# Performance work log

Measured on AMD Instinct MI355X. Metric: run time of the kernel, lower is better.

Reference implementation:

```python
import jax, jax.numpy as jnp
import numpy as np

DEPTH = 13                 # tree depth -> N = 2**DEPTH - 1 reaches (heap layout, outlet = node 0)
N = 2 ** DEPTH - 1         # 8191 reaches
T = 2048                   # timesteps


def setup_inputs() -> dict:
    key = jax.random.key(0)
    ks = jax.random.split(key, 8)
    u = lambda k, shape, lo, hi: jax.random.uniform(k, shape, minval=lo, maxval=hi, dtype=jnp.float32)
    return {
        "lateral_inflows": u(ks[0], (T, N), 0.0, 2.0),     # m^3/s lateral inflow per reach
        "manning_n":       u(ks[1], (N,), 0.025, 0.06),    # Manning roughness
        "lengths":         u(ks[2], (N,), 1000.0, 5000.0), # reach length [m]
        "slopes":          u(ks[3], (N,), 1e-4, 1e-2),     # bed slope (>= 1e-4 as in source)
        "width_coefs":     u(ks[4], (N,), 3.0, 10.0),      # w = wc * Q**we  (power-law geometry)
        "width_exps":      u(ks[5], (N,), 0.4, 0.6),
        "depth_coefs":     u(ks[6], (N,), 0.2, 0.5),       # h = dc * Q**de
        "depth_exps":      u(ks[7], (N,), 0.3, 0.45),
        "dt": 3600,                                        # routing timestep [s]
    }


def _mc_outflow(I_new, I_old, O_old, n, L, S, wc, we, dc, de, dt):
    """Variable-parameter Muskingum-Cunge update for one vector of reaches."""
    Qr = jnp.maximum(0.5 * (I_new + O_old), 1e-3)          # reference discharge
    h = dc * Qr ** de                                       # hydraulic depth
    w = wc * Qr ** we                                       # top width
    v = h ** (2.0 / 3.0) * jnp.sqrt(S) / n                  # Manning velocity
    c = jnp.maximum((5.0 / 3.0) * v, 1e-3)                  # kinematic celerity
    K = L / c                                               # travel time
    X = jnp.clip(0.5 * (1.0 - Qr / (w * S * c * L)), 0.0, 0.5)
    den = 2.0 * K * (1.0 - X) + dt
    C1 = (dt - 2.0 * K * X) / den
    C2 = (dt + 2.0 * K * X) / den
    C3 = (2.0 * K * (1.0 - X) - dt) / den
    return jnp.maximum(C1 * I_new + C2 * I_old + C3 * O_old, 0.0)


def reference(lateral_inflows, manning_n, lengths, slopes, width_coefs, width_exps,
              depth_coefs, depth_exps, dt):
    dtf = jnp.float32(dt)
    Np = lateral_inflows.shape[1]
    params = (manning_n, lengths, slopes, width_coefs, width_exps, depth_coefs, depth_exps)

    def step(carry, lat_t):
        I_old, O_old = carry                                # [N] prev inflow / outflow
        Q = jnp.zeros(Np, dtype=lat_t.dtype)                # new outflows this timestep
        I_all = jnp.zeros(Np, dtype=lat_t.dtype)
        # process levels leaves -> root (reverse topological order over the DAG)
        for l in range(DEPTH - 1, -1, -1):
            s, e = 2 ** l - 1, 2 ** (l + 1) - 1             # nodes of level l
            if l == DEPTH - 1:
                up = jnp.float32(0.0)                        # headwater reaches
            else:
                cs, ce = 2 ** (l + 1) - 1, 2 ** (l + 2) - 1  # children = level l+1
                up = Q[cs:ce:2] + Q[cs + 1:ce:2]             # sum of 2 upstream discharges
            I_new = lat_t[s:e] + up
            O_new = _mc_outflow(I_new, I_old[s:e], O_old[s:e],
                                *(p[s:e] for p in params), dtf)
            Q = Q.at[s:e].set(O_new)
            I_all = I_all.at[s:e].set(I_new)
        return (I_all, Q), Q[0]                              # outlet = root (index 0)

    init = (jnp.zeros(Np, jnp.float32), jnp.zeros(Np, jnp.float32))
    _, outlet_Q = jax.lax.scan(step, init, lateral_inflows)
    return outlet_Q                                          # [T]
```

## Files before the change

kernel.cpp:

```cpp
#include <hip/hip_runtime.h>


#define NN 8191
#define TT 2048
#define BATCH 32
#define NBLK 39
#define BTHREADS 256

#define FLAGS_FOFF 16773120ull
#define REQ_BYTES  67106816ull

#if __has_builtin(__builtin_amdgcn_exp2f)
__device__ __forceinline__ float fexp2(float x) { return __builtin_amdgcn_exp2f(x); }
#else
__device__ __forceinline__ float fexp2(float x) { return exp2f(x); }
#endif
#if __has_builtin(__builtin_amdgcn_logf)
__device__ __forceinline__ float flog2(float x) { return __builtin_amdgcn_logf(x); }
#else
__device__ __forceinline__ float flog2(float x) { return log2f(x); }
#endif
#if __has_builtin(__builtin_amdgcn_rcpf)
__device__ __forceinline__ float frcp(float x) { return __builtin_amdgcn_rcpf(x); }
#else
__device__ __forceinline__ float frcp(float x) { return 1.0f / x; }
#endif

__device__ __forceinline__ float mc_update(float Inew, float Iold, float Oold,
                                           float em, float tkc, float ex, float k1,
                                           float dtf)
{
    float Qr = fmaxf(0.5f * (Inew + Oold), 1e-3f);
    float lg = flog2(Qr);
    float twoK = tkc * fexp2(em * lg);
    float X = fmaxf(0.5f - k1 * fexp2(ex * lg), 0.0f);
    float A = twoK * X;
    float B = twoK - A;
    float r = frcp(B + dtf);
    float C1 = (dtf - A) * r;
    float C2 = (dtf + A) * r;
    float C3 = (B - dtf) * r;
    return fmaxf(C1 * Inew + C2 * Iold + C3 * Oold, 0.0f);
}

__constant__ int g_level[NBLK] = {
    12,12,12,12,12,12,12,12,12,12,12,12,12,12,12,12,
    11,11,11,11,11,11,11,11,
    10,10,10,10,
    9,9,
    8,7,6,5,4,3,2,1,0};
__constant__ int g_cnt[NBLK] = {
    256,256,256,256,256,256,256,256,256,256,256,256,256,256,256,256,
    256,256,256,256,256,256,256,256,
    256,256,256,256,
    256,256,
    256,128,64,32,16,8,4,2,1};
__constant__ int g_first[13] = {38,37,36,35,34,33,32,31,30,28,24,16,0};
__constant__ unsigned long long g_off[13] = {
    16773120ull, 16769024ull, 16760832ull, 16744448ull, 16711680ull,
    16646144ull, 16515072ull, 16252928ull, 15728640ull, 14680064ull,
    12582912ull, 8388608ull, 0ull};

#define FLAG_STRIDE 16

__device__ __forceinline__ void waitflags(const unsigned int* fa, const unsigned int* fb,
                                          unsigned int target)
{
    while (true) {
        unsigned int a = __hip_atomic_load(fa, __ATOMIC_RELAXED, __HIP_MEMORY_SCOPE_AGENT);
        unsigned int b = fb ? __hip_atomic_load(fb, __ATOMIC_RELAXED, __HIP_MEMORY_SCOPE_AGENT)
                            : a;
        if (a >= target && b >= target) break;
        __builtin_amdgcn_s_sleep(1);
    }
    __builtin_amdgcn_sched_barrier(0);
    asm volatile("" ::: "memory");
}

__global__ void zero_flags(unsigned int* flags)
{
    for (int i = threadIdx.x; i < NBLK * 4 * FLAG_STRIDE; i += 256) flags[i] = 0;
}

__global__ __launch_bounds__(BTHREADS)
void pipe_kernel(const float* __restrict__ lat,
                 const float* __restrict__ nman,
                 const float* __restrict__ len,
                 const float* __restrict__ slp,
                 const float* __restrict__ wcf,
                 const float* __restrict__ wex,
                 const float* __restrict__ dcf,
                 const float* __restrict__ dex,
                 const int*   __restrict__ dtp,
                 float*       __restrict__ out,
                 float*       __restrict__ ws)
{
    const int bid = blockIdx.x;
    const int tid = threadIdx.x;
    const int lvl = g_level[bid];
    const int cnt = g_cnt[bid];
    const int W   = tid >> 6;
    const int wn  = cnt - W * 64;
    if (wn <= 0) return;

    const bool active = (tid < cnt);
    const int B = bid - g_first[lvl];
    const int m = B * 256 + (active ? tid : 0);
    const int node = ((1 << lvl) - 1) + m;
    const int wbase = B * 256 + W * 64;

    unsigned int* flags = (unsigned int*)(ws + FLAGS_FOFF);
    unsigned int* myflag = flags + ((size_t)bid * 4 + W) * FLAG_STRIDE;

    const bool haschild = (lvl < 12);
    const unsigned int* fa = nullptr;
    const unsigned int* fb = nullptr;
    if (haschild) {
        const int Fp = g_first[lvl + 1];
        const int nw = wn < 64 ? wn : 64;
        const int p0 = (2 * wbase) >> 6;
        const int p1 = (2 * wbase + 2 * nw - 1) >> 6;
        fa = flags + ((size_t)(Fp + (p0 >> 2)) * 4 + (p0 & 3)) * FLAG_STRIDE;
        fb = (p1 != p0)
           ? flags + ((size_t)(Fp + (p1 >> 2)) * 4 + (p1 & 3)) * FLAG_STRIDE
           : nullptr;
    }

    const int myW = 1 << lvl;
    const int childW = 1 << (lvl + 1);
    float* myBuf = ws + g_off[lvl];
    const unsigned long long* childBuf =
        haschild ? (const unsigned long long*)(ws + g_off[lvl + 1]) : nullptr;

    const float dtf = (float)dtp[0];

    float em, tkc, ex, k1;
    float Iold = 0.0f, Oold = 0.0f;
    {
        float n = nman[node], L = len[node], S = slp[node];
        float wc = wcf[node], we = wex[node], dc = dcf[node], de = dex[node];
        float dc23 = fexp2(0.6666667f * flog2(dc));
        float cc = 1.6666667f * dc23 * sqrtf(S) * frcp(n);
        float e23 = 0.6666667f * de;
        em  = -e23;
        tkc = 2.0f * L * frcp(cc);
        ex  = 1.0f - we - e23;
        k1  = 0.5f * frcp(S * L * wc * cc);
    }

    for (int t0 = 0; t0 < TT; t0 += BATCH) {
        float la[BATCH];
        if (active) {
#pragma unroll
            for (int k = 0; k < BATCH; ++k)
                la[k] = lat[(size_t)(t0 + k) * NN + node];
        }

        if (haschild) waitflags(fa, fb, (unsigned int)(t0 + BATCH));

        if (active) {
            float c0[BATCH], c1[BATCH];
            if (haschild) {
#pragma unroll
                for (int k = 0; k < BATCH; ++k) {
                    unsigned long long cv = __hip_atomic_load(
                        childBuf + ((size_t)(t0 + k) * childW >> 1) + m,
                        __ATOMIC_RELAXED, __HIP_MEMORY_SCOPE_AGENT);
                    float2 c = *(float2*)&cv;
                    c0[k] = c.x; c1[k] = c.y;
                }
            }
#pragma unroll
            for (int k = 0; k < BATCH; ++k) {
                float Inew = la[k] + (haschild ? (c0[k] + c1[k]) : 0.0f);
                float O = mc_update(Inew, Iold, Oold, em, tkc, ex, k1, dtf);
                Iold = Inew; Oold = O;
                if (lvl > 0)
                    __hip_atomic_store(myBuf + (size_t)(t0 + k) * myW + m, O,
                                       __ATOMIC_RELAXED, __HIP_MEMORY_SCOPE_AGENT);
                else
                    out[t0 + k] = O;
            }
        }
        if (lvl > 0) {
            asm volatile("s_waitcnt vmcnt(0)" ::: "memory");
            if ((tid & 63) == 0)
                __hip_atomic_store(myflag, (unsigned int)(t0 + BATCH),
                                   __ATOMIC_RELAXED, __HIP_MEMORY_SCOPE_AGENT);
        }
    }
}

#define NTHREADS 1024
__global__ __launch_bounds__(NTHREADS)
void route_kernel(const float* __restrict__ lat,
                  const float* __restrict__ nman,
                  const float* __restrict__ len,
                  const float* __restrict__ slp,
                  const float* __restrict__ wcf,
                  const float* __restrict__ wex,
                  const float* __restrict__ dcf,
                  const float* __restrict__ dex,
                  const int*   __restrict__ dtp,
                  float*       __restrict__ out)
{
    __shared__ float Osh[NN];
    const int tid = threadIdx.x;
    const float dtf = (float)dtp[0];

    int nodes[8];
    nodes[0] = 4095 + tid;
    nodes[1] = 5119 + tid;
    nodes[2] = 6143 + tid;
    nodes[3] = 7167 + tid;
    nodes[4] = 2047 + tid;
    nodes[5] = 3071 + tid;
    nodes[6] = 1023 + tid;
    nodes[7] = (tid < 1023) ? tid : 0;

    float em[8], tkc[8], ex[8], k1[8];
    float Ireg[8], Oreg[8];
#pragma unroll
    for (int k = 0; k < 8; ++k) {
        int i = nodes[k];
        float n = nman[i], L = len[i], S = slp[i];
        float wc = wcf[i], we = wex[i], dc = dcf[i], de = dex[i];
        float dc23 = fexp2(0.6666667f * flog2(dc));
        float cc = 1.6666667f * dc23 * sqrtf(S) * frcp(n);
        float e23 = 0.6666667f * de;
        em[k]  = -e23;
        tkc[k] = 2.0f * L * frcp(cc);
        ex[k]  = 1.0f - we - e23;
        k1[k]  = 0.5f * frcp(S * L * wc * cc);
        Ireg[k] = 0.0f; Oreg[k] = 0.0f;
    }
    for (int i = tid; i < NN; i += NTHREADS) Osh[i] = 0.0f;
    __syncthreads();

    for (int t = 0; t < TT; ++t) {
        const float* __restrict__ latt = lat + (size_t)t * NN;
#pragma unroll
        for (int k = 0; k < 4; ++k) {
            int i = nodes[k];
            float Inew = latt[i];
            float O = mc_update(Inew, Ireg[k], Oreg[k], em[k], tkc[k], ex[k], k1[k], dtf);
            Ireg[k] = Inew; Oreg[k] = O; Osh[i] = O;
        }
        __syncthreads();
#pragma unroll
        for (int k = 4; k < 6; ++k) {
            int i = nodes[k];
            float Inew = latt[i] + Osh[2 * i + 1] + Osh[2 * i + 2];
            float O = mc_update(Inew, Ireg[k], Oreg[k], em[k], tkc[k], ex[k], k1[k], dtf);
            Ireg[k] = Inew; Oreg[k] = O; Osh[i] = O;
        }
        __syncthreads();
        {
            int i = nodes[6];
            float Inew = latt[i] + Osh[2 * i + 1] + Osh[2 * i + 2];
            float O = mc_update(Inew, Ireg[6], Oreg[6], em[6], tkc[6], ex[6], k1[6], dtf);
            Ireg[6] = Inew; Oreg[6] = O; Osh[i] = O;
        }
        __syncthreads();
        for (int l = 9; l >= 0; --l) {
            int s = (1 << l) - 1;
            int e = (1 << (l + 1)) - 1;
            if (tid >= s && tid < e) {
                int i = tid;
                float Inew = latt[i] + Osh[2 * i + 1] + Osh[2 * i + 2];
                float O = mc_update(Inew, Ireg[7], Oreg[7], em[7], tkc[7], ex[7], k1[7], dtf);
                Ireg[7] = Inew; Oreg[7] = O; Osh[i] = O;
            }
            __syncthreads();
        }
        if (tid == 0) out[t] = Oreg[7];
    }
}

extern "C" void kernel_launch(void* const* d_in, const int* in_sizes, int n_in,
                              void* d_out, int out_size, void* d_ws, size_t ws_size,
                              hipStream_t stream) {
    const float* lat  = (const float*)d_in[0];
    const float* nman = (const float*)d_in[1];
    const float* len  = (const float*)d_in[2];
    const float* slp  = (const float*)d_in[3];
    const float* wcf  = (const float*)d_in[4];
    const float* wex  = (const float*)d_in[5];
    const float* dcf  = (const float*)d_in[6];
    const float* dex  = (const float*)d_in[7];
    const int*   dtp  = (const int*)d_in[8];
    float* out = (float*)d_out;

    if (ws_size >= REQ_BYTES) {
        float* ws = (float*)d_ws;
        unsigned int* flags = (unsigned int*)(ws + FLAGS_FOFF);
        zero_flags<<<dim3(1), dim3(256), 0, stream>>>(flags);
        pipe_kernel<<<dim3(NBLK), dim3(BTHREADS), 0, stream>>>(
            lat, nman, len, slp, wcf, wex, dcf, dex, dtp, out, ws);
    } else {
        route_kernel<<<dim3(1), dim3(NTHREADS), 0, stream>>>(
            lat, nman, len, slp, wcf, wex, dcf, dex, dtp, out);
    }
}
```

Measured before the change: 483.5 us.

## Double-buffer lateral and child loads within larger flag batches in pipelined routing kernel

The level-pipelined kernel now waits on child flags once per 128 timesteps instead of every 32. Inside each batch it processes 16-step chunks and prefetches the next chunk's lateral and child values into alternate register buffers while computing the current one. The Muskingum-Cunge output is also rewritten algebraically to skip computing C1/C2/C3 separately. The larger batch cuts synchronization overhead but makes parent levels wait longer to start, which lengthens the pipeline fill across the 13 levels.

Measured after the change: 681.5 us. 1.41x slower.

```diff
diff --git a/kernel.cpp b/kernel.cpp
--- a/kernel.cpp
+++ b/kernel.cpp
@@ -3,12 +3,14 @@
 
 #define NN 8191
 #define TT 2048
-#define BATCH 32
+#define FBATCH 128
+#define CHUNK 16
 #define NBLK 39
 #define BTHREADS 256
 
 #define FLAGS_FOFF 16773120ull
 #define REQ_BYTES  67106816ull
+#define FLAG_STRIDE 16
 
 #if __has_builtin(__builtin_amdgcn_exp2f)
 __device__ __forceinline__ float fexp2(float x) { return __builtin_amdgcn_exp2f(x); }
@@ -25,23 +27,6 @@
 #else
 __device__ __forceinline__ float frcp(float x) { return 1.0f / x; }
 #endif
-
-__device__ __forceinline__ float mc_update(float Inew, float Iold, float Oold,
-                                           float em, float tkc, float ex, float k1,
-                                           float dtf)
-{
-    float Qr = fmaxf(0.5f * (Inew + Oold), 1e-3f);
-    float lg = flog2(Qr);
-    float twoK = tkc * fexp2(em * lg);
-    float X = fmaxf(0.5f - k1 * fexp2(ex * lg), 0.0f);
-    float A = twoK * X;
-    float B = twoK - A;
-    float r = frcp(B + dtf);
-    float C1 = (dtf - A) * r;
-    float C2 = (dtf + A) * r;
-    float C3 = (B - dtf) * r;
-    return fmaxf(C1 * Inew + C2 * Iold + C3 * Oold, 0.0f);
-}
 
 __constant__ int g_level[NBLK] = {
     12,12,12,12,12,12,12,12,12,12,12,12,12,12,12,12,
@@ -61,8 +46,6 @@
     16646144ull, 16515072ull, 16252928ull, 15728640ull, 14680064ull,
     12582912ull, 8388608ull, 0ull};
 
-#define FLAG_STRIDE 16
-
 __device__ __forceinline__ void waitflags(const unsigned int* fa, const unsigned int* fb,
                                           unsigned int target)
 {
@@ -148,50 +131,98 @@
         k1  = 0.5f * frcp(S * L * wc * cc);
     }
 
-    for (int t0 = 0; t0 < TT; t0 += BATCH) {
-        float la[BATCH];
-        if (active) {
-#pragma unroll
-            for (int k = 0; k < BATCH; ++k)
-                la[k] = lat[(size_t)(t0 + k) * NN + node];
-        }
-
-        if (haschild) waitflags(fa, fb, (unsigned int)(t0 + BATCH));
-
-        if (active) {
-            float c0[BATCH], c1[BATCH];
-            if (haschild) {
-#pragma unroll
-                for (int k = 0; k < BATCH; ++k) {
-                    unsigned long long cv = __hip_atomic_load(
-                        childBuf + ((size_t)(t0 + k) * childW >> 1) + m,
-                        __ATOMIC_RELAXED, __HIP_MEMORY_SCOPE_AGENT);
-                    float2 c = *(float2*)&cv;
-                    c0[k] = c.x; c1[k] = c.y;
-                }
-            }
-#pragma unroll
-            for (int k = 0; k < BATCH; ++k) {
-                float Inew = la[k] + (haschild ? (c0[k] + c1[k]) : 0.0f);
-                float O = mc_update(Inew, Iold, Oold, em, tkc, ex, k1, dtf);
-                Iold = Inew; Oold = O;
-                if (lvl > 0)
-                    __hip_atomic_store(myBuf + (size_t)(t0 + k) * myW + m, O,
-                                       __ATOMIC_RELAXED, __HIP_MEMORY_SCOPE_AGENT);
-                else
-                    out[t0 + k] = O;
-            }
-        }
+    float laA[CHUNK], c0A[CHUNK], c1A[CHUNK];
+    float laB[CHUNK], c0B[CHUNK], c1B[CHUNK];
+
+#define LLOAD(buf, tb)                                                        \
+    if (active) {                                                             \
+        _Pragma("unroll")                                                     \
+        for (int k = 0; k < CHUNK; ++k)                                       \
+            buf[k] = lat[(size_t)((tb) + k) * NN + node];                     \
+    }
+
+#define CLOAD(b0, b1, tb)                                                     \
+    if (haschild && active) {                                                 \
+        _Pragma("unroll")                                                     \
+        for (int k = 0; k < CHUNK; ++k) {                                     \
+            unsigned long long cv = __hip_atomic_load(                        \
+                childBuf + ((size_t)((tb) + k) * childW >> 1) + m,            \
+                __ATOMIC_RELAXED, __HIP_MEMORY_SCOPE_AGENT);                  \
+            float2 c = *(float2*)&cv;                                         \
+            b0[k] = c.x; b1[k] = c.y;                                         \
+        }                                                                     \
+    }
+
+#define COMP(la, b0, b1, tb)                                                  \
+    if (active) {                                                             \
+        _Pragma("unroll")                                                     \
+        for (int k = 0; k < CHUNK; ++k) {                                     \
+            float Inew = la[k] + (haschild ? (b0[k] + b1[k]) : 0.0f);         \
+            float Qr = fmaxf(0.5f * (Inew + Oold), 1e-3f);                    \
+            float lg = flog2(Qr);                                             \
+            float twoK = tkc * fexp2(em * lg);                                \
+            float X = fmaxf(0.5f - k1 * fexp2(ex * lg), 0.0f);                \
+            float A = twoK * X;                                               \
+            float Bv = twoK - A;                                              \
+            float r = frcp(Bv + dtf);                                         \
+            float num = dtf * (Inew + Iold - Oold) + A * (Iold - Inew)        \
+                      + Bv * Oold;                                            \
+            float O = fmaxf(num * r, 0.0f);                                   \
+            Iold = Inew; Oold = O;                                            \
+            if (lvl > 0)                                                      \
+                __hip_atomic_store(myBuf + (size_t)((tb) + k) * myW + m, O,   \
+                                   __ATOMIC_RELAXED, __HIP_MEMORY_SCOPE_AGENT);\
+            else                                                              \
+                out[(tb) + k] = O;                                            \
+        }                                                                     \
+    }
+
+    LLOAD(laA, 0);
+
+    for (int t0 = 0; t0 < TT; t0 += FBATCH) {
+        if (haschild) waitflags(fa, fb, (unsigned int)(t0 + FBATCH));
+
+        CLOAD(c0A, c1A, t0);
+        LLOAD(laB, t0 + 16);  CLOAD(c0B, c1B, t0 + 16);  COMP(laA, c0A, c1A, t0);
+        LLOAD(laA, t0 + 32);  CLOAD(c0A, c1A, t0 + 32);  COMP(laB, c0B, c1B, t0 + 16);
+        LLOAD(laB, t0 + 48);  CLOAD(c0B, c1B, t0 + 48);  COMP(laA, c0A, c1A, t0 + 32);
+        LLOAD(laA, t0 + 64);  CLOAD(c0A, c1A, t0 + 64);  COMP(laB, c0B, c1B, t0 + 48);
+        LLOAD(laB, t0 + 80);  CLOAD(c0B, c1B, t0 + 80);  COMP(laA, c0A, c1A, t0 + 64);
+        LLOAD(laA, t0 + 96);  CLOAD(c0A, c1A, t0 + 96);  COMP(laB, c0B, c1B, t0 + 80);
+        LLOAD(laB, t0 + 112); CLOAD(c0B, c1B, t0 + 112); COMP(laA, c0A, c1A, t0 + 96);
+        COMP(laB, c0B, c1B, t0 + 112);
+
         if (lvl > 0) {
             asm volatile("s_waitcnt vmcnt(0)" ::: "memory");
             if ((tid & 63) == 0)
-                __hip_atomic_store(myflag, (unsigned int)(t0 + BATCH),
+                __hip_atomic_store(myflag, (unsigned int)(t0 + FBATCH),
                                    __ATOMIC_RELAXED, __HIP_MEMORY_SCOPE_AGENT);
         }
-    }
+        if (t0 + FBATCH < TT) { LLOAD(laA, t0 + FBATCH); }
+    }
+#undef LLOAD
+#undef CLOAD
+#undef COMP
 }
 
 #define NTHREADS 1024
+__device__ __forceinline__ float mc_update_fb(float Inew, float Iold, float Oold,
+                                              float em, float tkc, float ex, float k1,
+                                              float dtf)
+{
+    float Qr = fmaxf(0.5f * (Inew + Oold), 1e-3f);
+    float lg = flog2(Qr);
+    float twoK = tkc * fexp2(em * lg);
+    float X = fmaxf(0.5f - k1 * fexp2(ex * lg), 0.0f);
+    float A = twoK * X;
+    float B = twoK - A;
+    float r = frcp(B + dtf);
+    float C1 = (dtf - A) * r;
+    float C2 = (dtf + A) * r;
+    float C3 = (B - dtf) * r;
+    return fmaxf(C1 * Inew + C2 * Iold + C3 * Oold, 0.0f);
+}
+
 __global__ __launch_bounds__(NTHREADS)
 void route_kernel(const float* __restrict__ lat,
                   const float* __restrict__ nman,
@@ -243,7 +274,7 @@
         for (int k = 0; k < 4; ++k) {
             int i = nodes[k];
             float Inew = latt[i];
-            float O = mc_update(Inew, Ireg[k], Oreg[k], em[k], tkc[k], ex[k], k1[k], dtf);
+            float O = mc_update_fb(Inew, Ireg[k], Oreg[k], em[k], tkc[k], ex[k], k1[k], dtf);
             Ireg[k] = Inew; Oreg[k] = O; Osh[i] = O;
         }
         __syncthreads();
@@ -251,14 +282,14 @@
         for (int k = 4; k < 6; ++k) {
             int i = nodes[k];
             float Inew = latt[i] + Osh[2 * i + 1] + Osh[2 * i + 2];
-            float O = mc_update(Inew, Ireg[k], Oreg[k], em[k], tkc[k], ex[k], k1[k], dtf);
+            float O = mc_update_fb(Inew, Ireg[k], Oreg[k], em[k], tkc[k], ex[k], k1[k], dtf);
             Ireg[k] = Inew; Oreg[k] = O; Osh[i] = O;
         }
         __syncthreads();
         {
             int i = nodes[6];
             float Inew = latt[i] + Osh[2 * i + 1] + Osh[2 * i + 2];
-            float O = mc_update(Inew, Ireg[6], Oreg[6], em[6], tkc[6], ex[6], k1[6], dtf);
+            float O = mc_update_fb(Inew, Ireg[6], Oreg[6], em[6], tkc[6], ex[6], k1[6], dtf);
             Ireg[6] = Inew; Oreg[6] = O; Osh[i] = O;
         }
         __syncthreads();
@@ -268,7 +299,7 @@
             if (tid >= s && tid < e) {
                 int i = tid;
                 float Inew = latt[i] + Osh[2 * i + 1] + Osh[2 * i + 2];
-                float O = mc_update(Inew, Ireg[7], Oreg[7], em[7], tkc[7], ex[7], k1[7], dtf);
+                float O = mc_update_fb(Inew, Ireg[7], Oreg[7], em[7], tkc[7], ex[7], k1[7], dtf);
                 Ireg[7] = Inew; Oreg[7] = O; Osh[i] = O;
             }
             __syncthreads();
```
